# Optimization experiments

Hardware: AMD Instinct MI355X
Metric: run time of the kernel (lower is better)

Reference implementation:

```python
import jax, jax.numpy as jnp
import numpy as np

BN_EPS = 1e-5
W_SCALE = 0.05  # keep pre-softmax logits in a sane range with random weights


def setup_inputs() -> dict:
    key = jax.random.key(0)
    ks = jax.random.split(key, 8)
    b, C, H, W = 2, 512, 80, 80
    Ck, Cv, Co = 256, 256, 512
    return {
        "x": jax.random.normal(ks[0], (b, C, H, W), dtype=jnp.float32),
        "wk": jax.random.normal(ks[1], (Ck, C), dtype=jnp.float32) * W_SCALE,
        "bk": jax.random.normal(ks[2], (Ck,), dtype=jnp.float32) * W_SCALE,
        "gamma": jnp.ones((Ck,), dtype=jnp.float32),
        "beta": jnp.zeros((Ck,), dtype=jnp.float32),
        "rmean": jnp.zeros((Ck,), dtype=jnp.float32),
        "rvar": jnp.ones((Ck,), dtype=jnp.float32),
        "wv": jax.random.normal(ks[3], (Cv, C), dtype=jnp.float32) * W_SCALE,
        "bv": jax.random.normal(ks[4], (Cv,), dtype=jnp.float32) * W_SCALE,
        "wW": jax.random.normal(ks[5], (Co, Cv), dtype=jnp.float32) * W_SCALE,
        "bW": jax.random.normal(ks[6], (Co,), dtype=jnp.float32) * W_SCALE,
    }


def reference(x, wk, bk, gamma, beta, rmean, rvar, wv, bv, wW, bW):
    b, C, H, Wd = x.shape
    N = H * Wd
    Ck = wk.shape[0]
    Cv = wv.shape[0]
    # f_key == f_query (shared module): 1x1 conv + BN(inference) + ReLU
    k = jnp.einsum('bchw,oc->bohw', x, wk) + bk[:, None, None]
    scale_bn = gamma / jnp.sqrt(rvar + BN_EPS)
    k = (k - rmean[:, None, None]) * scale_bn[:, None, None] + beta[:, None, None]
    k = jax.nn.relu(k).reshape(b, Ck, N)          # [b, Ck, N]
    q = jnp.transpose(k, (0, 2, 1))               # [b, N, Ck] (query shares weights with key)
    # f_value: plain 1x1 conv
    v = (jnp.einsum('bchw,oc->bohw', x, wv) + bv[:, None, None]).reshape(b, Cv, N)
    sim = jnp.einsum('bnc,bcm->bnm', q, k) * (Ck ** -0.5)  # [b, N, N]
    sim = jax.nn.softmax(sim, axis=-1)
    ctx = jnp.einsum('bnm,bvm->bvn', sim, v).reshape(b, Cv, H, Wd)
    out = jnp.einsum('bvhw,ov->bohw', ctx, wW) + bW[:, None, None]
    return out
```

## Files before the change

### kernel.cpp

```cpp
#include <hip/hip_runtime.h>
#include <stdint.h>

typedef __attribute__((ext_vector_type(8))) short bf16x8;
typedef __attribute__((ext_vector_type(4))) float f32x4;

__device__ __forceinline__ float bf2f(ushort u) {
    union { uint32_t i; float f; } v; v.i = ((uint32_t)u) << 16; return v.f;
}
__device__ __forceinline__ ushort f2bf(float f) {
    union { float f; uint32_t i; } v; v.f = f;
    uint32_t r = v.i + 0x7fff + ((v.i >> 16) & 1);
    return (ushort)(r >> 16);
}

typedef unsigned int uint_as1 __attribute__((address_space(1)));
typedef unsigned int uint_as3 __attribute__((address_space(3)));
__device__ __forceinline__ void async16(const void* g, void* l) {
    __builtin_amdgcn_global_load_lds((const uint_as1*)g, (uint_as3*)l, 16, 0, 0);
}


__global__ void cvt_f32_bf16(const float* __restrict__ in, ushort* __restrict__ out, int n) {
    int i = blockIdx.x * blockDim.x + threadIdx.x;
    if (i < n) out[i] = f2bf(in[i]);
}

__global__ void prep_bn(const float* __restrict__ bk, const float* __restrict__ gamma,
                        const float* __restrict__ beta, const float* __restrict__ rmean,
                        const float* __restrict__ rvar,
                        float* __restrict__ scaleA, float* __restrict__ shiftA) {
    int i = threadIdx.x;
    float s = gamma[i] * rsqrtf(rvar[i] + 1e-5f);
    scaleA[i] = 0.25f * s;
    shiftA[i] = 0.25f * ((bk[i] - rmean[i]) * s + beta[i]);
}

__global__ void transpose_cvt(const float* __restrict__ x, ushort* __restrict__ xt) {
    __shared__ float t[32][33];
    int b = blockIdx.z;
    int n0 = blockIdx.x * 32, c0 = blockIdx.y * 32;
    const float* xb = x + (size_t)b * 512 * 6400;
    ushort* xtb = xt + (size_t)b * 6400 * 512;
    int tx = threadIdx.x, ty = threadIdx.y;
    t[ty][tx] = xb[(size_t)(c0 + ty) * 6400 + n0 + tx];
    __syncthreads();
    xtb[(size_t)(n0 + ty) * 512 + c0 + tx] = f2bf(t[tx][ty]);
}

template <int EPI>
__global__ __launch_bounds__(256) void gemm_nt(
    const ushort* __restrict__ A, const ushort* __restrict__ B, void* __restrict__ Cout,
    int K, int lda, int ldb, int ldc,
    size_t zsa, size_t zsb, size_t zsc,
    const float* __restrict__ vec0, const float* __restrict__ vec1,
    float* __restrict__ rsum) {
    __shared__ __align__(16) ushort smem[4 * 4096];

    A += (size_t)blockIdx.z * zsa;
    B += (size_t)blockIdx.z * zsb;

    const int tid = threadIdx.x;
    const int lane = tid & 63, wave = tid >> 6;
    const int wm = wave & 1, wn = wave >> 1;
    const int bM = blockIdx.y * 128, bN = blockIdx.x * 128;

    const int sr = lane >> 2;
    const int sc = (lane & 3) * 8;
    const ushort* gA0 = A + (size_t)(bM + wave * 32 + sr) * lda + sc;
    const ushort* gA1 = gA0 + (size_t)16 * lda;
    const ushort* gB0 = B + (size_t)(bN + wave * 32 + sr) * ldb + sc;
    const ushort* gB1 = gB0 + (size_t)16 * ldb;
    ushort* lAw = &smem[wave * 1024];
    ushort* lBw = &smem[2 * 4096 + wave * 1024];

    const int rowA = wm * 64;
    const int rowB = wn * 64;
    const int fr = lane & 15;
    const int fk = (lane >> 4) * 8;

    f32x4 acc[4][4] = {};
    const int nT = K >> 5;

    async16(gA0, lAw);
    async16(gA1, lAw + 512);
    async16(gB0, lBw);
    async16(gB1, lBw + 512);
    __syncthreads();

    int cur = 0;
    for (int t = 0; t < nT; ++t) {
        if (t + 1 < nT) {
            const int k0 = (t + 1) * 32;
            const int nb = (cur ^ 1) * 4096;
            async16(gA0 + k0, lAw + nb);
            async16(gA1 + k0, lAw + nb + 512);
            async16(gB0 + k0, lBw + nb);
            async16(gB1 + k0, lBw + nb + 512);
        }
        const ushort* lA = &smem[cur * 4096];
        const ushort* lB = &smem[2 * 4096 + cur * 4096];
        bf16x8 af[4], bff[4];
#pragma unroll
        for (int mi = 0; mi < 4; mi++)
            af[mi] = *(const bf16x8*)&lA[(rowA + mi * 16 + fr) * 32 + fk];
#pragma unroll
        for (int ni = 0; ni < 4; ni++)
            bff[ni] = *(const bf16x8*)&lB[(rowB + ni * 16 + fr) * 32 + fk];
#pragma unroll
        for (int mi = 0; mi < 4; mi++)
#pragma unroll
            for (int ni = 0; ni < 4; ni++)
                acc[mi][ni] = __builtin_amdgcn_mfma_f32_16x16x32_bf16(af[mi], bff[ni], acc[mi][ni], 0, 0, 0);
        __syncthreads();
        cur ^= 1;
    }

    float* Cf = (float*)Cout + (size_t)blockIdx.z * zsc;
    ushort* Cu = (ushort*)Cout + (size_t)blockIdx.z * zsc;
    float* lt = (float*)smem;
    const int g4 = (lane >> 4) * 4;
    const int cl = lane & 15;
    const int lr = tid >> 3;
    const int ch = tid & 7;

#pragma unroll
    for (int mi = 0; mi < 4; ++mi) {
#pragma unroll
        for (int ni = 0; ni < 4; ++ni) {
            const int lcol = wn * 64 + ni * 16 + cl;
#pragma unroll
            for (int r = 0; r < 4; ++r)
                lt[(wm * 16 + g4 + r) * 132 + lcol] = acc[mi][ni][r];
        }
        __syncthreads();
        {
            const int brow = (lr < 16) ? (mi * 16 + lr) : (64 + mi * 16 + (lr - 16));
            const int grow = bM + brow;
            const int gcol = bN + ch * 16;
            float vv[16];
#pragma unroll
            for (int i = 0; i < 16; i += 4) {
                f32x4 q = *(const f32x4*)&lt[lr * 132 + ch * 16 + i];
                vv[i] = q[0]; vv[i + 1] = q[1]; vv[i + 2] = q[2]; vv[i + 3] = q[3];
            }
            if (EPI == 1) {
#pragma unroll
                for (int i = 0; i < 16; i++)
                    vv[i] = fmaxf(vv[i] * vec0[gcol + i] + vec1[gcol + i], 0.f);
            }
            if (EPI == 2 || EPI == 3) {
                const float rb = vec0[grow];
#pragma unroll
                for (int i = 0; i < 16; i++) vv[i] += rb;
            }
            if (EPI == 5) {
                float ssum = 0.f;
#pragma unroll
                for (int i = 0; i < 16; i++) { vv[i] = __expf(vv[i]); ssum += vv[i]; }
                ssum += __shfl_down(ssum, 4, 8);
                ssum += __shfl_down(ssum, 2, 8);
                ssum += __shfl_down(ssum, 1, 8);
                if (ch == 0) rsum[(size_t)blockIdx.x * 6400 + grow] = ssum;
            }
            if (EPI == 3 || EPI == 4) {
#pragma unroll
                for (int i = 0; i < 16; i += 4) {
                    f32x4 q = { vv[i], vv[i + 1], vv[i + 2], vv[i + 3] };
                    *(f32x4*)&Cf[(size_t)grow * ldc + gcol + i] = q;
                }
            } else {
                ushort o16[16];
#pragma unroll
                for (int i = 0; i < 16; i++) o16[i] = f2bf(vv[i]);
                *(uint4*)&Cu[(size_t)grow * ldc + gcol] = *(const uint4*)&o16[0];
                *(uint4*)&Cu[(size_t)grow * ldc + gcol + 8] = *(const uint4*)&o16[8];
            }
        }
        __syncthreads();
    }
}

__global__ __launch_bounds__(256) void combine_inv(const float* __restrict__ rsum,
                                                   float* __restrict__ inv) {
    int r = blockIdx.x * 256 + threadIdx.x;
    float s = 0.f;
#pragma unroll
    for (int xb = 0; xb < 50; xb++) s += rsum[(size_t)xb * 6400 + r];
    inv[r] = 1.f / s;
}

__global__ __launch_bounds__(256) void reduce_ctx(const float* __restrict__ part, ushort* __restrict__ ctx,
                                                  const float* __restrict__ inv) {
    const size_t CH = 1638400;
    size_t i = ((size_t)blockIdx.x * 256 + threadIdx.x) * 4;
    float4 a = *(const float4*)&part[i];
#pragma unroll
    for (int c = 1; c < 5; c++) {
        float4 s = *(const float4*)&part[i + (size_t)c * CH];
        a.x += s.x; a.y += s.y; a.z += s.z; a.w += s.w;
    }
    const float w = inv[i >> 8];
    ushort o[4];
    o[0] = f2bf(a.x * w);
    o[1] = f2bf(a.y * w);
    o[2] = f2bf(a.z * w);
    o[3] = f2bf(a.w * w);
    *(uint2*)&ctx[i] = *(const uint2*)o;
}

extern "C" void kernel_launch(void* const* d_in, const int* in_sizes, int n_in,
                              void* d_out, int out_size, void* d_ws, size_t ws_size,
                              hipStream_t stream) {
    (void)in_sizes; (void)n_in; (void)out_size; (void)ws_size;
    const float* x     = (const float*)d_in[0];
    const float* wk    = (const float*)d_in[1];
    const float* bk    = (const float*)d_in[2];
    const float* gamma = (const float*)d_in[3];
    const float* beta  = (const float*)d_in[4];
    const float* rmean = (const float*)d_in[5];
    const float* rvar  = (const float*)d_in[6];
    const float* wv    = (const float*)d_in[7];
    const float* bv    = (const float*)d_in[8];
    const float* wW    = (const float*)d_in[9];
    const float* bW    = (const float*)d_in[10];
    float* out = (float*)d_out;

    ushort* Xt   = (ushort*)d_ws;
    ushort* wkb  = Xt + 6553600;
    ushort* wvb  = wkb + 131072;
    ushort* wWb  = wvb + 131072;
    ushort* Kt   = wWb + 131072;
    ushort* V    = Kt + 3276800;
    ushort* ctxT = V + 3276800;
    ushort* S    = ctxT + 3276800;
    float* scaleA = (float*)(S + 40960000);
    float* shiftA = scaleA + 256;
    float* rowsum = shiftA + 256;
    float* inv    = rowsum + 320000;
    float* part   = inv + 6400;

    cvt_f32_bf16<<<512, 256, 0, stream>>>(wk, wkb, 131072);
    cvt_f32_bf16<<<512, 256, 0, stream>>>(wv, wvb, 131072);
    cvt_f32_bf16<<<512, 256, 0, stream>>>(wW, wWb, 131072);
    prep_bn<<<1, 256, 0, stream>>>(bk, gamma, beta, rmean, rvar, scaleA, shiftA);
    transpose_cvt<<<dim3(200, 16, 2), dim3(32, 32), 0, stream>>>(x, Xt);

    gemm_nt<1><<<dim3(2, 50, 2), 256, 0, stream>>>(Xt, wkb, Kt, 512, 512, 512, 256,
                                                   3276800, 0, 1638400, scaleA, shiftA, nullptr);
    gemm_nt<2><<<dim3(50, 2, 2), 256, 0, stream>>>(wvb, Xt, V, 512, 512, 512, 6400,
                                                   0, 3276800, 1638400, bv, nullptr, nullptr);

    for (int b = 0; b < 2; b++) {
        ushort* Ktb  = Kt + (size_t)b * 1638400;
        ushort* Vb   = V  + (size_t)b * 1638400;
        ushort* ctxb = ctxT + (size_t)b * 1638400;
        gemm_nt<5><<<dim3(50, 50), 256, 0, stream>>>(Ktb, Ktb, S, 256, 256, 256, 6400,
                                                     0, 0, 0, nullptr, nullptr, rowsum);
        combine_inv<<<25, 256, 0, stream>>>(rowsum, inv);
        gemm_nt<4><<<dim3(2, 50, 5), 256, 0, stream>>>(S, Vb, part, 1280, 6400, 6400, 256,
                                                       1280, 1280, 1638400, nullptr, nullptr, nullptr);
        reduce_ctx<<<1600, 256, 0, stream>>>(part, ctxb, inv);
    }

    gemm_nt<3><<<dim3(50, 4, 2), 256, 0, stream>>>(wWb, ctxT, out, 256, 256, 256, 6400,
                                                   0, 1638400, 3276800, bW, nullptr, nullptr);
}
```

Measured before the change: 319.1 us.

## Triple-buffer GEMM LDS staging with explicit vmcnt waits and prefetch distance two

Replaces the double-buffered LDS pipeline in the bf16 MFMA GEMM with a three-slot ring. Loads run two K-tiles ahead, and only the oldest tile's global-to-LDS loads are waited on via s_waitcnt vmcnt(4). A single barrier per iteration replaces the trailing __syncthreads. This is meant to hide global load latency behind MFMA work, at the cost of 50% more shared memory, which may reduce occupancy.

```diff
diff --git a/kernel.cpp b/kernel.cpp
--- a/kernel.cpp
+++ b/kernel.cpp
@@ -54,7 +54,7 @@
     size_t zsa, size_t zsb, size_t zsc,
     const float* __restrict__ vec0, const float* __restrict__ vec1,
     float* __restrict__ rsum) {
-    __shared__ __align__(16) ushort smem[4 * 4096];
+    __shared__ __align__(16) ushort smem[6 * 4096];
 
     A += (size_t)blockIdx.z * zsa;
     B += (size_t)blockIdx.z * zsb;
@@ -71,7 +71,7 @@
     const ushort* gB0 = B + (size_t)(bN + wave * 32 + sr) * ldb + sc;
     const ushort* gB1 = gB0 + (size_t)16 * ldb;
     ushort* lAw = &smem[wave * 1024];
-    ushort* lBw = &smem[2 * 4096 + wave * 1024];
+    ushort* lBw = &smem[3 * 4096 + wave * 1024];
 
     const int rowA = wm * 64;
     const int rowB = wn * 64;
@@ -81,24 +81,28 @@
     f32x4 acc[4][4] = {};
     const int nT = K >> 5;
 
-    async16(gA0, lAw);
-    async16(gA1, lAw + 512);
-    async16(gB0, lBw);
-    async16(gB1, lBw + 512);
-    __syncthreads();
-
-    int cur = 0;
+    auto stage = [&](int t, int buf) {
+        const int k0 = t * 32;
+        const int ob = buf * 4096;
+        async16(gA0 + k0, lAw + ob);
+        async16(gA1 + k0, lAw + ob + 512);
+        async16(gB0 + k0, lBw + ob);
+        async16(gB1 + k0, lBw + ob + 512);
+    };
+
+    stage(0, 0);
+    if (nT > 1) stage(1, 1);
+
     for (int t = 0; t < nT; ++t) {
-        if (t + 1 < nT) {
-            const int k0 = (t + 1) * 32;
-            const int nb = (cur ^ 1) * 4096;
-            async16(gA0 + k0, lAw + nb);
-            async16(gA1 + k0, lAw + nb + 512);
-            async16(gB0 + k0, lBw + nb);
-            async16(gB1 + k0, lBw + nb + 512);
-        }
+        if (t + 1 < nT) { asm volatile("s_waitcnt vmcnt(4)" ::: "memory"); }
+        else            { asm volatile("s_waitcnt vmcnt(0)" ::: "memory"); }
+        __builtin_amdgcn_sched_barrier(0);
+        __builtin_amdgcn_s_barrier();
+        __builtin_amdgcn_sched_barrier(0);
+        if (t + 2 < nT) stage(t + 2, (t + 2) % 3);
+        const int cur = t % 3;
         const ushort* lA = &smem[cur * 4096];
-        const ushort* lB = &smem[2 * 4096 + cur * 4096];
+        const ushort* lB = &smem[3 * 4096 + cur * 4096];
         bf16x8 af[4], bff[4];
 #pragma unroll
         for (int mi = 0; mi < 4; mi++)
@@ -111,9 +115,10 @@
 #pragma unroll
             for (int ni = 0; ni < 4; ni++)
                 acc[mi][ni] = __builtin_amdgcn_mfma_f32_16x16x32_bf16(af[mi], bff[ni], acc[mi][ni], 0, 0, 0);
-        __syncthreads();
-        cur ^= 1;
-    }
+        __builtin_amdgcn_sched_barrier(0);
+    }
+    __builtin_amdgcn_s_barrier();
+    __builtin_amdgcn_sched_barrier(0);
 
     float* Cf = (float*)Cout + (size_t)blockIdx.z * zsc;
     ushort* Cu = (ushort*)Cout + (size_t)blockIdx.z * zsc;
```

Result: no change. 314.6 us (-1.4%).
